# Kernel optimization log

Hardware: AMD Instinct MI355X
Metric: run time of the kernel (lower is better)

## Reference

```python
import jax, jax.numpy as jnp
import numpy as np

N, CIO, L = 16, 512, 384
DIMHEAD, NUMHEAD, MAXEMBED, DIMGROUP = 64, 8, 384, 8
CHID = DIMHEAD * NUMHEAD


def setup_inputs() -> dict:
    key = jax.random.key(0)
    ks = jax.random.split(key, 12)
    s = 0.05
    return {
        "x": jax.random.normal(ks[0], (N, CIO, L), jnp.float32),
        "xorg": jax.random.normal(ks[1], (N, CIO, L), jnp.float32),
        "abspos": jax.random.normal(ks[2], (N, CIO, L), jnp.float32),
        "mask": jnp.zeros((N, L), jnp.float32),
        "norm": jnp.full((N,), 8.0, jnp.float32),
        "qkpos_res": s * jax.random.normal(ks[3], (CIO // DIMGROUP, 1), jnp.float32),
        "qkorg_res": s * jax.random.normal(ks[4], (CIO // DIMGROUP, 1), jnp.float32),
        "vorg_res": s * jax.random.normal(ks[5], (CIO // DIMGROUP, 1), jnp.float32),
        "relpos": s * jax.random.normal(ks[6], (2 * MAXEMBED - 1,), jnp.float32),
        "gate_w": s * jax.random.normal(ks[7], (NUMHEAD, CIO), jnp.float32),
        "gate_b": jnp.zeros((NUMHEAD,), jnp.float32),
        "q_w": s * jax.random.normal(ks[8], (CHID, CIO), jnp.float32),
        "k_w": s * jax.random.normal(ks[9], (CHID, CIO), jnp.float32),
        "v_w": s * jax.random.normal(ks[10], (CHID, CIO), jnp.float32),
        "dense_w": s * jax.random.normal(ks[11], (CIO, CHID), jnp.float32),
        "dense_b": jnp.zeros((CIO,), jnp.float32),
    }


def _rezero(t, res):
    # (N,C,L) -> reshape to (N, C//DIMGROUP, DIMGROUP*L), scale per group, reshape back
    n, c, l = t.shape
    return (t.reshape(n, c // DIMGROUP, -1) * res).reshape(n, c, l)


def _relpos_idx():
    # idx[i, j] = clip(MAXEMBED - i + j, 0, 2*MAXEMBED - 2)
    idx = np.arange(MAXEMBED, MAXEMBED - L, -1)[:, None] + np.arange(L)[None, :]
    return jnp.asarray(np.clip(idx, 0, 2 * MAXEMBED - 2))


def reference(x, xorg, abspos, mask, norm, qkpos_res, qkorg_res, vorg_res,
              relpos, gate_w, gate_b, q_w, k_w, v_w, dense_w, dense_b):
    n = x.shape[0]
    x0 = x + _rezero(xorg, vorg_res)                     # value path
    x1 = x + _rezero(xorg, qkorg_res) + _rezero(abspos, qkpos_res)  # qk path

    q = jnp.einsum('oc,ncl->nol', q_w, x1).reshape(n, NUMHEAD, DIMHEAD, L)
    k = jnp.einsum('oc,ncl->nol', k_w, x1).reshape(n, NUMHEAD, DIMHEAD, L)
    v = jnp.einsum('oc,ncl->nol', v_w, x0).reshape(n, NUMHEAD, DIMHEAD, L)

    scores = jnp.einsum('nhdi,nhdj->nhij', q, k)         # (N, H, L, L)
    gate = jnp.einsum('oc,ncl->nol', gate_w, x) + gate_b[None, :, None]  # (N, H, L)
    scores = (scores + relpos[_relpos_idx()]
              + gate[:, :, None, :]
              + mask[:, None, None, :]) / norm[:, None, None, None]

    attn = jax.nn.softmax(scores, axis=-1)
    out = jnp.einsum('nhij,nhdj->nhdi', attn, v).reshape(n, CHID, L)
    out = jnp.einsum('oc,ncl->nol', dense_w, out) + dense_b[None, :, None]
    return out
```

## Files before the change

kernel.cpp:

```cpp
#include <hip/hip_runtime.h>
#include <hip/hip_bf16.h>

#define N_B   16
#define CIO   512
#define LSEQ  384
#define DH    64
#define NH    8
#define CHID  512
#define ME    384

typedef __hip_bfloat16 bf16;
typedef __attribute__((ext_vector_type(8))) short bf16x8;
typedef __attribute__((ext_vector_type(4))) float f32x4;

#define AS1 __attribute__((address_space(1)))
#define AS3 __attribute__((address_space(3)))

__device__ __forceinline__ unsigned short f2bs(float f) {
    union { bf16 b; unsigned short u; } cv; cv.b = __float2bfloat16(f); return cv.u;
}

__device__ __forceinline__ void gload_lds16(const bf16* g, bf16* l) {
    __builtin_amdgcn_global_load_lds((const AS1 unsigned int*)g,
                                     (AS3 unsigned int*)l, 16, 0, 0);
}

__launch_bounds__(256)
__global__ void prep_kernel(const float* __restrict__ x, const float* __restrict__ xorg,
                            const float* __restrict__ abspos,
                            const float* __restrict__ qkorg, const float* __restrict__ qkpos,
                            const float* __restrict__ vorg,
                            const float* __restrict__ gw,
                            const float* __restrict__ q_w, const float* __restrict__ k_w,
                            const float* __restrict__ v_w, const float* __restrict__ dense_w,
                            bf16* __restrict__ wqb, bf16* __restrict__ wkb,
                            bf16* __restrict__ wvb, bf16* __restrict__ wdb,
                            bf16* __restrict__ x1t, bf16* __restrict__ x0t,
                            float* __restrict__ gpart)
{
    __shared__ bf16 T1[64 * 72], T0[64 * 72];
    __shared__ float Traw[64 * 65];
    __shared__ float gws[NH * 64];
    __shared__ float r0[64], r1[64], r2[64];
    const int tid = threadIdx.x;
    const int cb = blockIdx.x;
    const int c0 = cb * 64;
    const int l0 = blockIdx.y * 64;
    const int n  = blockIdx.z;

    {
        int f = blockIdx.x + 8 * (blockIdx.y + 6 * blockIdx.z);
        if (f < 512) {
            int e = (f * 256 + tid) * 8;
            int which = e >> 18;
            int off = e & ((1 << 18) - 1);
            const float* s = which == 0 ? q_w : which == 1 ? k_w : which == 2 ? v_w : dense_w;
            bf16* d       = which == 0 ? wqb : which == 1 ? wkb : which == 2 ? wvb : wdb;
            float4 f0 = *(const float4*)&s[off];
            float4 f1 = *(const float4*)&s[off + 4];
            unsigned short u[8] = {f2bs(f0.x), f2bs(f0.y), f2bs(f0.z), f2bs(f0.w),
                                   f2bs(f1.x), f2bs(f1.y), f2bs(f1.z), f2bs(f1.w)};
            *(uint4*)&d[off] = *(uint4*)u;
        }
    }

    if (tid < 64) {
        int gidx = (c0 + tid) >> 3;
        r0[tid] = vorg[gidx];
        r1[tid] = qkorg[gidx];
        r2[tid] = qkpos[gidx];
    }
    for (int t = tid; t < NH * 64; t += 256) {
        int h = t >> 6, c = t & 63;
        gws[t] = gw[h * CIO + c0 + c];
    }
    __syncthreads();
    const int l = tid & 63, cs = tid >> 6;
    #pragma unroll
    for (int r = 0; r < 16; r++) {
        int cl = r * 4 + cs;
        size_t gi = ((size_t)n * CIO + c0 + cl) * LSEQ + l0 + l;
        float xv = x[gi], xo = xorg[gi];
        Traw[cl * 65 + l] = xv;
        T0[l * 72 + cl] = __float2bfloat16(xv + r0[cl] * xo);
        T1[l * 72 + cl] = __float2bfloat16(xv + r1[cl] * xo + r2[cl] * abspos[gi]);
    }
    __syncthreads();
    for (int t = tid; t < NH * 64; t += 256) {
        int h = t >> 6, ll = t & 63;
        float s = 0.f;
        #pragma unroll
        for (int c = 0; c < 64; c++) s += gws[h * 64 + c] * Traw[c * 65 + ll];
        gpart[(((size_t)cb * N_B + n) * NH + h) * LSEQ + l0 + ll] = s;
    }
    #pragma unroll
    for (int t = 0; t < 2; t++) {
        int idx = t * 256 + tid;
        int lr = idx >> 3, u = idx & 7;
        size_t go = ((size_t)n * LSEQ + l0 + lr) * CIO + c0 + u * 8;
        *(uint4*)&x1t[go] = *(const uint4*)&T1[lr * 72 + u * 8];
        *(uint4*)&x0t[go] = *(const uint4*)&T0[lr * 72 + u * 8];
    }
}

__launch_bounds__(256)
__global__ void qkv_kernel(const bf16* __restrict__ wall,
                           const bf16* __restrict__ x1t, const bf16* __restrict__ x0t,
                           bf16* __restrict__ qb, bf16* __restrict__ kb,
                           bf16* __restrict__ vb)
{
    __shared__ __align__(16) char smem[17408];
    bf16* As = (bf16*)smem;
    bf16* Bs = (bf16*)(smem + 8192);
    bf16* S  = (bf16*)smem;

    const int tid = threadIdx.x;
    const int lane = tid & 63, w = tid >> 6;
    const int l15 = lane & 15, g = lane >> 4;
    const int Bid = blockIdx.x;
    const int rres = Bid & 7, qq = Bid >> 3;
    const int n = rres + 8 * (qq / 36);
    const int t = qq % 36;
    const int ot = t / 3;
    const int lt = t % 3;
    const int osub = (w & 1) * 64, lsub = (w >> 1) * 64;

    const bf16* Wt = wall + (size_t)(ot * 128) * CIO;
    const bf16* Bt = (ot < 8 ? x1t : x0t) + ((size_t)n * LSEQ + lt * 128) * CIO;

    const int segA = 2 * w, segB = 2 * w + 1;
    const int eA = segA * 512 + lane * 8;
    const int eB = segB * 512 + lane * 8;
    const int rA = eA >> 5, cA = eA & 31;
    const int rB = eB >> 5, cB = eB & 31;

    f32x4 acc[4][4];
    #pragma unroll
    for (int mt = 0; mt < 4; mt++)
        #pragma unroll
        for (int jt = 0; jt < 4; jt++) acc[mt][jt] = f32x4{0.f, 0.f, 0.f, 0.f};

    for (int it = 0; it < 16; ++it) {
        const int k0 = it * 32;
        gload_lds16(Wt + (size_t)rA * CIO + k0 + cA, As + segA * 512);
        gload_lds16(Wt + (size_t)rB * CIO + k0 + cB, As + segB * 512);
        gload_lds16(Bt + (size_t)rA * CIO + k0 + cA, Bs + segA * 512);
        gload_lds16(Bt + (size_t)rB * CIO + k0 + cB, Bs + segB * 512);
        __syncthreads();
        bf16x8 af[4], bfv[4];
        #pragma unroll
        for (int mt = 0; mt < 4; mt++)
            af[mt] = *(const bf16x8*)&As[(osub + mt * 16 + l15) * 32 + 8 * g];
        #pragma unroll
        for (int jt = 0; jt < 4; jt++)
            bfv[jt] = *(const bf16x8*)&Bs[(lsub + jt * 16 + l15) * 32 + 8 * g];
        #pragma unroll
        for (int mt = 0; mt < 4; mt++)
            #pragma unroll
            for (int jt = 0; jt < 4; jt++)
                acc[mt][jt] = __builtin_amdgcn_mfma_f32_16x16x32_bf16(af[mt], bfv[jt], acc[mt][jt], 0, 0, 0);
        __syncthreads();
    }

    if (ot < 8) {
        bf16* dstb = (ot < 4) ? qb : kb;
        const int hbase = 2 * (ot & 3);
        #pragma unroll
        for (int lh = 0; lh < 2; ++lh) {
            if ((w >> 1) == lh) {
                #pragma unroll
                for (int mt = 0; mt < 4; mt++)
                    #pragma unroll
                    for (int jt = 0; jt < 4; jt++)
                        #pragma unroll
                        for (int r = 0; r < 4; r++)
                            S[(jt * 16 + l15) * 136 + osub + mt * 16 + 4 * g + r] =
                                __float2bfloat16(acc[mt][jt][r]);
            }
            __syncthreads();
            #pragma unroll
            for (int t2 = 0; t2 < 4; ++t2) {
                int idx = t2 * 256 + tid;
                int lr = idx >> 4, u = idx & 15;
                int ho = u >> 3, dc = u & 7;
                bf16* dst = dstb + (((size_t)n * NH + hbase + ho) * LSEQ
                                    + lt * 128 + lh * 64 + lr) * DH + dc * 8;
                *(uint4*)dst = *(const uint4*)&S[lr * 136 + u * 8];
            }
            __syncthreads();
        }
    } else {
        const int ob = (ot - 8) * 128;
        #pragma unroll
        for (int oh = 0; oh < 2; ++oh) {
            if ((w & 1) == oh) {
                #pragma unroll
                for (int mt = 0; mt < 4; mt++)
                    #pragma unroll
                    for (int jt = 0; jt < 4; jt++)
                        #pragma unroll
                        for (int r = 0; r < 4; r++)
                            S[(mt * 16 + 4 * g + r) * 136 + lsub + jt * 16 + l15] =
                                __float2bfloat16(acc[mt][jt][r]);
            }
            __syncthreads();
            #pragma unroll
            for (int t2 = 0; t2 < 4; ++t2) {
                int idx = t2 * 256 + tid;
                int orr = idx >> 4, u = idx & 15;
                bf16* dst = vb + ((size_t)(n * CHID + ob + oh * 64 + orr)) * LSEQ
                               + lt * 128 + u * 8;
                *(uint4*)dst = *(const uint4*)&S[orr * 136 + u * 8];
            }
            __syncthreads();
        }
    }
}

__launch_bounds__(256, 3)
__global__ void attn_kernel(const bf16* __restrict__ qt,
                            const bf16* __restrict__ kt,
                            const bf16* __restrict__ v,
                            const float* __restrict__ gpart,
                            const float* __restrict__ gb,
                            const float* __restrict__ mask,
                            const float* __restrict__ norm,
                            const float* __restrict__ relpos,
                            bf16* __restrict__ ctxt)
{
    __shared__ __align__(16) char smem[25600];
    __shared__ float relp_s[2 * ME - 1];
    __shared__ float radd_s[LSEQ];

    bf16* P = (bf16*)smem;
    bf16* O = (bf16*)smem;

    const int tid = threadIdx.x;
    const int Bid = blockIdx.x;
    const int rres = Bid & 7, qq = Bid >> 3;
    const int n = rres + 8 * (qq / 48);
    const int rem = qq % 48;
    const int h = rem / 6;
    const int i0 = (rem % 6) * 64;
    const int lane = tid & 63;
    const int w = tid >> 6;
    const int l15 = lane & 15, g = lane >> 4;
    const int m0 = w * 16;

    const size_t nh = (size_t)n * NH + h;
    const bf16* kt_g = kt + nh * LSEQ * DH;
    const bf16* vg   = v + ((size_t)n * CHID + h * DH) * LSEQ;

    {
        const float gbh = gb[h];
        for (int i = tid; i < LSEQ; i += 256) {
            float s = gbh + mask[(size_t)n * LSEQ + i];
            #pragma unroll
            for (int cb = 0; cb < 8; cb++)
                s += gpart[(((size_t)cb * N_B + n) * NH + h) * LSEQ + i];
            radd_s[i] = s;
        }
    }
    for (int i = tid; i < 2 * ME - 1; i += 256) relp_s[i] = relpos[i];

    const bf16* qrow = qt + (nh * LSEQ + i0 + m0 + l15) * DH;
    bf16x8 a0 = *(const bf16x8*)&qrow[8 * g];
    bf16x8 a1 = *(const bf16x8*)&qrow[8 * g + 32];
    const float inv_norm = 1.0f / norm[n];
    __syncthreads();

    const int ib = i0 + m0 + 4 * g;
    f32x4 oacc[4];
    #pragma unroll
    for (int dn = 0; dn < 4; dn++) oacc[dn] = f32x4{0.f, 0.f, 0.f, 0.f};
    float m_r[4]  = {-1e30f, -1e30f, -1e30f, -1e30f};
    float lsum[4] = {0.f, 0.f, 0.f, 0.f};

    #pragma unroll
    for (int half = 0; half < 2; half++) {
        const int j0 = half * 192;

        f32x4 acc[12];
        #pragma unroll
        for (int jt = 0; jt < 12; jt++) acc[jt] = f32x4{0.f, 0.f, 0.f, 0.f};
        #pragma unroll
        for (int jt = 0; jt < 12; jt++) {
            const bf16* kr = &kt_g[(size_t)(j0 + jt * 16 + l15) * DH + 8 * g];
            bf16x8 b0 = *(const bf16x8*)kr;
            bf16x8 b1 = *(const bf16x8*)(kr + 32);
            acc[jt] = __builtin_amdgcn_mfma_f32_16x16x32_bf16(a0, b0, acc[jt], 0, 0, 0);
            acc[jt] = __builtin_amdgcn_mfma_f32_16x16x32_bf16(a1, b1, acc[jt], 0, 0, 0);
        }

        float mx[4] = {-1e30f, -1e30f, -1e30f, -1e30f};
        #pragma unroll
        for (int jt = 0; jt < 12; jt++) {
            float ra = radd_s[j0 + jt * 16 + l15];
            #pragma unroll
            for (int r = 0; r < 4; r++) {
                int idx = ME - (ib + r) + j0 + jt * 16 + l15;
                idx = (idx > 2 * ME - 2) ? (2 * ME - 2) : idx;
                float s = (acc[jt][r] + relp_s[idx] + ra) * inv_norm;
                acc[jt][r] = s;
                mx[r] = fmaxf(mx[r], s);
            }
        }
        #pragma unroll
        for (int r = 0; r < 4; r++) {
            #pragma unroll
            for (int off = 1; off <= 8; off <<= 1)
                mx[r] = fmaxf(mx[r], __shfl_xor(mx[r], off));
            float mnew = fmaxf(m_r[r], mx[r]);
            float sc = __expf(m_r[r] - mnew);
            m_r[r] = mnew;
            lsum[r] *= sc;
            #pragma unroll
            for (int dn = 0; dn < 4; dn++) oacc[dn][r] *= sc;
        }
        #pragma unroll
        for (int jt = 0; jt < 12; jt++) {
            #pragma unroll
            for (int r = 0; r < 4; r++) {
                float e = __expf(acc[jt][r] - m_r[r]);
                lsum[r] += e;
                P[(m0 + 4 * g + r) * 200 + jt * 16 + l15] = __float2bfloat16(e);
            }
        }

        bf16x8 vreg[2][4];
        #pragma unroll
        for (int dn = 0; dn < 4; dn++)
            vreg[0][dn] = *(const bf16x8*)&vg[(size_t)(dn * 16 + l15) * LSEQ + j0 + 8 * g];
        #pragma unroll
        for (int jt2 = 0; jt2 < 6; jt2++) {
            const int s = jt2 & 1;
            if (jt2 < 5) {
                #pragma unroll
                for (int dn = 0; dn < 4; dn++)
                    vreg[s ^ 1][dn] = *(const bf16x8*)&vg[(size_t)(dn * 16 + l15) * LSEQ + j0 + (jt2 + 1) * 32 + 8 * g];
            }
            bf16x8 a = *(const bf16x8*)&P[(m0 + l15) * 200 + jt2 * 32 + 8 * g];
            #pragma unroll
            for (int dn = 0; dn < 4; dn++)
                oacc[dn] = __builtin_amdgcn_mfma_f32_16x16x32_bf16(a, vreg[s][dn], oacc[dn], 0, 0, 0);
        }
    }

    float rs[4];
    #pragma unroll
    for (int r = 0; r < 4; r++) {
        float t = lsum[r];
        #pragma unroll
        for (int off = 1; off <= 8; off <<= 1) t += __shfl_xor(t, off);
        rs[r] = 1.0f / t;
    }

    __syncthreads();
    #pragma unroll
    for (int dn = 0; dn < 4; dn++)
        #pragma unroll
        for (int r = 0; r < 4; r++)
            O[(m0 + 4 * g + r) * 72 + dn * 16 + l15] = __float2bfloat16(oacc[dn][r] * rs[r]);
    __syncthreads();

    bf16* cg_ = ctxt + ((size_t)n * LSEQ + i0) * CHID + h * DH;
    #pragma unroll
    for (int t = 0; t < 2; t++) {
        int idx = t * 256 + tid;
        int ir = idx >> 3, u = idx & 7;
        *(uint4*)&cg_[(size_t)ir * CHID + u * 8] = *(const uint4*)&O[ir * 72 + u * 8];
    }
}

__launch_bounds__(256, 6)
__global__ void dense_kernel(const bf16* __restrict__ Wb,
                             const bf16* __restrict__ Bt,
                             const float* __restrict__ bias,
                             float* __restrict__ outf)
{
    __shared__ __align__(16) float S[64 * 68];
    const int tid = threadIdx.x;
    const int lane = tid & 63, w = tid >> 6;
    const int l15 = lane & 15, g = lane >> 4;
    const int Bid = blockIdx.x;
    const int rres = Bid & 7, qq = Bid >> 3;
    const int n = rres + 8 * (qq / 48);
    const int tt = qq % 48;
    const int o0 = (tt / 6) * 64;
    const int l0 = (tt % 6) * 64;

    const bf16* arow = Wb + (size_t)(o0 + l15) * CIO + 8 * g;
    const bf16* brow = Bt + ((size_t)n * LSEQ + l0 + w * 16 + l15) * CIO + 8 * g;

    f32x4 acc[4];
    #pragma unroll
    for (int mt = 0; mt < 4; mt++) acc[mt] = f32x4{0.f, 0.f, 0.f, 0.f};
    #pragma unroll 4
    for (int it = 0; it < 16; it++) {
        const int k0 = it * 32;
        bf16x8 b = *(const bf16x8*)&brow[k0];
        bf16x8 a[4];
        #pragma unroll
        for (int mt = 0; mt < 4; mt++)
            a[mt] = *(const bf16x8*)&arow[(size_t)mt * 16 * CIO + k0];
        #pragma unroll
        for (int mt = 0; mt < 4; mt++)
            acc[mt] = __builtin_amdgcn_mfma_f32_16x16x32_bf16(a[mt], b, acc[mt], 0, 0, 0);
    }

    #pragma unroll
    for (int mt = 0; mt < 4; mt++)
        #pragma unroll
        for (int r = 0; r < 4; r++)
            S[(mt * 16 + 4 * g + r) * 68 + w * 16 + l15] =
                acc[mt][r] + bias[o0 + mt * 16 + 4 * g + r];
    __syncthreads();
    float* og = outf + ((size_t)n * CHID + o0) * LSEQ + l0;
    #pragma unroll
    for (int t = 0; t < 4; t++) {
        int idx = t * 256 + tid;
        int orow = idx >> 4, u = idx & 15;
        *(float4*)&og[(size_t)orow * LSEQ + u * 4] = *(const float4*)&S[orow * 68 + u * 4];
    }
}

extern "C" void kernel_launch(void* const* d_in, const int* in_sizes, int n_in,
                              void* d_out, int out_size, void* d_ws, size_t ws_size,
                              hipStream_t stream)
{
    const float* x       = (const float*)d_in[0];
    const float* xorg    = (const float*)d_in[1];
    const float* abspos  = (const float*)d_in[2];
    const float* mask    = (const float*)d_in[3];
    const float* norm    = (const float*)d_in[4];
    const float* qkpos   = (const float*)d_in[5];
    const float* qkorg   = (const float*)d_in[6];
    const float* vorg    = (const float*)d_in[7];
    const float* relpos  = (const float*)d_in[8];
    const float* gate_w  = (const float*)d_in[9];
    const float* gate_b  = (const float*)d_in[10];
    const float* q_w     = (const float*)d_in[11];
    const float* k_w     = (const float*)d_in[12];
    const float* v_w     = (const float*)d_in[13];
    const float* dense_w = (const float*)d_in[14];
    const float* dense_b = (const float*)d_in[15];
    float* out = (float*)d_out;

    const size_t TEN = (size_t)N_B * CHID * LSEQ * sizeof(bf16);
    const size_t WB  = (size_t)CHID * CIO * sizeof(bf16);
    char* ws = (char*)d_ws;
    bf16*  x1t  = (bf16*)(ws);
    bf16*  x0t  = (bf16*)(ws + TEN);
    bf16*  qb   = (bf16*)(ws + 2 * TEN);
    bf16*  kb   = (bf16*)(ws + 3 * TEN);
    bf16*  vb   = (bf16*)(ws + 4 * TEN);
    bf16*  wqb  = (bf16*)(ws + 5 * TEN);
    bf16*  wkb  = (bf16*)(ws + 5 * TEN + WB);
    bf16*  wvb  = (bf16*)(ws + 5 * TEN + 2 * WB);
    bf16*  wdb  = (bf16*)(ws + 5 * TEN + 3 * WB);
    float* gpart = (float*)(ws + 5 * TEN + 4 * WB);
    bf16*  ctxt = x1t;

    prep_kernel<<<dim3(CIO / 64, LSEQ / 64, N_B), 256, 0, stream>>>(
        x, xorg, abspos, qkorg, qkpos, vorg, gate_w,
        q_w, k_w, v_w, dense_w, wqb, wkb, wvb, wdb, x1t, x0t, gpart);
    qkv_kernel<<<576, 256, 0, stream>>>(wqb, x1t, x0t, qb, kb, vb);
    attn_kernel<<<768, 256, 0, stream>>>(qb, kb, vb, gpart, gate_b,
                                         mask, norm, relpos, ctxt);
    dense_kernel<<<768, 256, 0, stream>>>(wdb, ctxt, dense_b, out);
}
```

Before: 197.6 us.

## Stream K/V tiles through double-buffered swizzled LDS in attention kernel

The attention kernel now walks the key/value sequence in 64-wide tiles instead of two 192-wide halves. Each tile of K and V is loaded once per block into LDS with direct global-to-LDS loads, and the next tile is prefetched into a second buffer while the current one is used. An XOR swizzle is applied to K, V and a per-wave P buffer to avoid LDS bank conflicts. This removes the redundant per-wave global reads of K and V, but adds one block barrier per tile, uses more LDS, and shortens the online-softmax chunks, so rescaling happens more often.

```diff
diff --git a/kernel.cpp b/kernel.cpp
--- a/kernel.cpp
+++ b/kernel.cpp
@@ -217,6 +217,9 @@
     }
 }
 
+#define KVT 64
+#define NT  (LSEQ / KVT)
+
 __launch_bounds__(256, 3)
 __global__ void attn_kernel(const bf16* __restrict__ qt,
                             const bf16* __restrict__ kt,
@@ -228,12 +231,11 @@
                             const float* __restrict__ relpos,
                             bf16* __restrict__ ctxt)
 {
-    __shared__ __align__(16) char smem[25600];
+    __shared__ __align__(16) bf16 Kb[2][KVT * DH];
+    __shared__ __align__(16) bf16 Vb[2][KVT * DH];
+    __shared__ __align__(16) bf16 P[4 * 16 * 64];
     __shared__ float relp_s[2 * ME - 1];
     __shared__ float radd_s[LSEQ];
-
-    bf16* P = (bf16*)smem;
-    bf16* O = (bf16*)smem;
 
     const int tid = threadIdx.x;
     const int Bid = blockIdx.x;
@@ -267,38 +269,62 @@
     bf16x8 a0 = *(const bf16x8*)&qrow[8 * g];
     bf16x8 a1 = *(const bf16x8*)&qrow[8 * g + 32];
     const float inv_norm = 1.0f / norm[n];
+
+    const int c0_ = (2 * w) * 64 + lane;
+    const int c1_ = (2 * w + 1) * 64 + lane;
+    const int kr0 = c0_ >> 3, kc0 = ((c0_ & 7) ^ (kr0 & 7)) * 8;
+    const int kr1 = c1_ >> 3, kc1 = ((c1_ & 7) ^ (kr1 & 7)) * 8;
+    const int koff0 = kr0 * DH + kc0, koff1 = kr1 * DH + kc1;
+    const int voff0 = kr0 * LSEQ + kc0, voff1 = kr1 * LSEQ + kc1;
+
+    gload_lds16(kt_g + koff0, &Kb[0][(2 * w) * 512]);
+    gload_lds16(kt_g + koff1, &Kb[0][(2 * w + 1) * 512]);
+    gload_lds16(vg + voff0, &Vb[0][(2 * w) * 512]);
+    gload_lds16(vg + voff1, &Vb[0][(2 * w + 1) * 512]);
     __syncthreads();
 
     const int ib = i0 + m0 + 4 * g;
+    bf16* Pw = P + w * 1024;
+
     f32x4 oacc[4];
     #pragma unroll
     for (int dn = 0; dn < 4; dn++) oacc[dn] = f32x4{0.f, 0.f, 0.f, 0.f};
     float m_r[4]  = {-1e30f, -1e30f, -1e30f, -1e30f};
     float lsum[4] = {0.f, 0.f, 0.f, 0.f};
 
-    #pragma unroll
-    for (int half = 0; half < 2; half++) {
-        const int j0 = half * 192;
-
-        f32x4 acc[12];
-        #pragma unroll
-        for (int jt = 0; jt < 12; jt++) acc[jt] = f32x4{0.f, 0.f, 0.f, 0.f};
-        #pragma unroll
-        for (int jt = 0; jt < 12; jt++) {
-            const bf16* kr = &kt_g[(size_t)(j0 + jt * 16 + l15) * DH + 8 * g];
-            bf16x8 b0 = *(const bf16x8*)kr;
-            bf16x8 b1 = *(const bf16x8*)(kr + 32);
+    #pragma unroll 2
+    for (int t = 0; t < NT; ++t) {
+        const int cur = t & 1;
+        if (t + 1 < NT) {
+            const bf16* kn = kt_g + (t + 1) * (KVT * DH);
+            const bf16* vn = vg + (t + 1) * KVT;
+            gload_lds16(kn + koff0, &Kb[cur ^ 1][(2 * w) * 512]);
+            gload_lds16(kn + koff1, &Kb[cur ^ 1][(2 * w + 1) * 512]);
+            gload_lds16(vn + voff0, &Vb[cur ^ 1][(2 * w) * 512]);
+            gload_lds16(vn + voff1, &Vb[cur ^ 1][(2 * w + 1) * 512]);
+        }
+
+        f32x4 acc[4];
+        #pragma unroll
+        for (int jt = 0; jt < 4; jt++) acc[jt] = f32x4{0.f, 0.f, 0.f, 0.f};
+        #pragma unroll
+        for (int jt = 0; jt < 4; jt++) {
+            const int row = jt * 16 + l15;
+            bf16x8 b0 = *(const bf16x8*)&Kb[cur][row * 64 + ((g ^ (row & 7)) * 8)];
+            bf16x8 b1 = *(const bf16x8*)&Kb[cur][row * 64 + (((4 + g) ^ (row & 7)) * 8)];
             acc[jt] = __builtin_amdgcn_mfma_f32_16x16x32_bf16(a0, b0, acc[jt], 0, 0, 0);
             acc[jt] = __builtin_amdgcn_mfma_f32_16x16x32_bf16(a1, b1, acc[jt], 0, 0, 0);
         }
 
         float mx[4] = {-1e30f, -1e30f, -1e30f, -1e30f};
         #pragma unroll
-        for (int jt = 0; jt < 12; jt++) {
-            float ra = radd_s[j0 + jt * 16 + l15];
+        for (int jt = 0; jt < 4; jt++) {
+            const int j = t * KVT + jt * 16 + l15;
+            const float ra = radd_s[j];
+            const int idxb = ME - ib + j;
             #pragma unroll
             for (int r = 0; r < 4; r++) {
-                int idx = ME - (ib + r) + j0 + jt * 16 + l15;
+                int idx = idxb - r;
                 idx = (idx > 2 * ME - 2) ? (2 * ME - 2) : idx;
                 float s = (acc[jt][r] + relp_s[idx] + ra) * inv_norm;
                 acc[jt][r] = s;
@@ -318,44 +344,40 @@
             for (int dn = 0; dn < 4; dn++) oacc[dn][r] *= sc;
         }
         #pragma unroll
-        for (int jt = 0; jt < 12; jt++) {
+        for (int jt = 0; jt < 4; jt++) {
+            const int col = jt * 16 + l15;
             #pragma unroll
             for (int r = 0; r < 4; r++) {
+                const int lr = 4 * g + r;
                 float e = __expf(acc[jt][r] - m_r[r]);
                 lsum[r] += e;
-                P[(m0 + 4 * g + r) * 200 + jt * 16 + l15] = __float2bfloat16(e);
-            }
-        }
-
-        bf16x8 vreg[2][4];
-        #pragma unroll
-        for (int dn = 0; dn < 4; dn++)
-            vreg[0][dn] = *(const bf16x8*)&vg[(size_t)(dn * 16 + l15) * LSEQ + j0 + 8 * g];
-        #pragma unroll
-        for (int jt2 = 0; jt2 < 6; jt2++) {
-            const int s = jt2 & 1;
-            if (jt2 < 5) {
-                #pragma unroll
-                for (int dn = 0; dn < 4; dn++)
-                    vreg[s ^ 1][dn] = *(const bf16x8*)&vg[(size_t)(dn * 16 + l15) * LSEQ + j0 + (jt2 + 1) * 32 + 8 * g];
-            }
-            bf16x8 a = *(const bf16x8*)&P[(m0 + l15) * 200 + jt2 * 32 + 8 * g];
-            #pragma unroll
-            for (int dn = 0; dn < 4; dn++)
-                oacc[dn] = __builtin_amdgcn_mfma_f32_16x16x32_bf16(a, vreg[s][dn], oacc[dn], 0, 0, 0);
-        }
+                Pw[lr * 64 + (col ^ ((lr & 7) << 3))] = __float2bfloat16(e);
+            }
+        }
+
+        #pragma unroll
+        for (int kh = 0; kh < 2; kh++) {
+            bf16x8 a = *(const bf16x8*)&Pw[l15 * 64 + (((kh * 4 + g) ^ (l15 & 7)) * 8)];
+            #pragma unroll
+            for (int dn = 0; dn < 4; dn++) {
+                const int vr = dn * 16 + l15;
+                bf16x8 bv = *(const bf16x8*)&Vb[cur][vr * 64 + (((kh * 4 + g) ^ (vr & 7)) * 8)];
+                oacc[dn] = __builtin_amdgcn_mfma_f32_16x16x32_bf16(a, bv, oacc[dn], 0, 0, 0);
+            }
+        }
+        __syncthreads();
     }
 
     float rs[4];
     #pragma unroll
     for (int r = 0; r < 4; r++) {
-        float t = lsum[r];
-        #pragma unroll
-        for (int off = 1; off <= 8; off <<= 1) t += __shfl_xor(t, off);
-        rs[r] = 1.0f / t;
-    }
-
-    __syncthreads();
+        float tm = lsum[r];
+        #pragma unroll
+        for (int off = 1; off <= 8; off <<= 1) tm += __shfl_xor(tm, off);
+        rs[r] = 1.0f / tm;
+    }
+
+    bf16* O = &Kb[0][0];
     #pragma unroll
     for (int dn = 0; dn < 4; dn++)
         #pragma unroll
```

Result: faster. 178.7 us (median of 2 runs) (-9.6%).
